# Kernel tuning notes

Measured on AMD Instinct MI355X. Metric: run time of the kernel, lower is better.

## Reference

```python
import jax, jax.numpy as jnp
from jax import lax
import numpy as np

DN = ('NCDHW', 'OIDHW', 'NCDHW')
SLOPE = 0.01   # nn.LeakyReLU default negative_slope
EPS = 1e-5     # nn.BatchNorm1d default eps


def _conv(x, w, s, p):
    return lax.conv_general_dilated(x, w, (s, s, s), [(p, p)] * 3,
                                    dimension_numbers=DN)


def _tconv(x, w):
    # ConvTranspose3d(k=4, s=2, p=1) == conv with lhs_dilation=2,
    # pad = k-1-p = 2, spatially flipped kernel. w is (C_out, C_in, 4,4,4).
    return lax.conv_general_dilated(x, jnp.flip(w, (2, 3, 4)), (1, 1, 1),
                                    [(2, 2)] * 3, lhs_dilation=(2, 2, 2),
                                    dimension_numbers=DN)


def _bcast(v):
    return v[None, :, None, None, None]


def _masked_bn(y, m, g, b):
    # BatchNorm1d over ACTIVE voxels only (spconv stores only active sites).
    cnt = jnp.maximum(jnp.sum(m), 1.0)
    mean = jnp.sum(y * m, axis=(0, 2, 3, 4)) / cnt
    var = jnp.sum(jnp.square(y - _bcast(mean)) * m, axis=(0, 2, 3, 4)) / cnt
    yhat = (y - _bcast(mean)) * _bcast(lax.rsqrt(var + EPS))
    return (yhat * _bcast(g) + _bcast(b)) * m


def _block(x, m, w, b, g, be, transpose):
    # spconv SparseConv(Transpose)3d -> LeakyReLU -> BatchNorm1d, emulated
    # densely: x is zero off the active set m; output active set is the
    # dilation of m by the kernel footprint; bias/activation/BN touch only
    # active sites.
    ones_k = jnp.ones((1, 1, 4, 4, 4), x.dtype)
    if transpose:
        y = _tconv(x, w)
        m2 = (_tconv(m, ones_k) > 0).astype(x.dtype)
    else:
        y = _conv(x, w, 2, 1)
        m2 = (_conv(m, ones_k, 2, 1) > 0).astype(x.dtype)
    y = (y + _bcast(b)) * m2
    y = jnp.where(y >= 0, y, SLOPE * y)  # LeakyReLU (preserves zeros)
    return _masked_bn(y, m2, g, be), m2


def setup_inputs() -> dict:
    key = jax.random.key(0)
    ks = jax.random.split(key, 16)
    B, C, D = 2, 4, 64
    c = 32          # chans
    pred_dim = 32

    def w_init(k, shape):
        scale = 1.0 / float(np.sqrt(np.prod(shape[1:])))
        return jax.random.normal(k, shape, jnp.float32) * scale

    def b_init(k, n):
        return jax.random.normal(k, (n,), jnp.float32) * 0.01

    inp = {
        'feat': jax.random.normal(ks[0], (B, C, D, D, D), jnp.float32),
        'mask': jax.random.uniform(ks[1], (B, 1, D, D, D), jnp.float32),
        # down: [C->c, c->2c, 2c->4c], k=4 s=2 p=1
        'w1': w_init(ks[2], (c, C, 4, 4, 4)),
        'b1': b_init(ks[3], c),
        'g1': jnp.ones((c,), jnp.float32), 'be1': jnp.zeros((c,), jnp.float32),
        'w2': w_init(ks[4], (2 * c, c, 4, 4, 4)),
        'b2': b_init(ks[5], 2 * c),
        'g2': jnp.ones((2 * c,), jnp.float32), 'be2': jnp.zeros((2 * c,), jnp.float32),
        'w3': w_init(ks[6], (4 * c, 2 * c, 4, 4, 4)),
        'b3': b_init(ks[7], 4 * c),
        'g3': jnp.ones((4 * c,), jnp.float32), 'be3': jnp.zeros((4 * c,), jnp.float32),
        # up: [4c->4c, 4c->2c] (no skip-concat in the executed forward)
        'tw1': w_init(ks[8], (4 * c, 4 * c, 4, 4, 4)),
        'tb1': b_init(ks[9], 4 * c),
        'tg1': jnp.ones((4 * c,), jnp.float32), 'tbe1': jnp.zeros((4 * c,), jnp.float32),
        'tw2': w_init(ks[10], (2 * c, 4 * c, 4, 4, 4)),
        'tb2': b_init(ks[11], 2 * c),
        'tg2': jnp.ones((2 * c,), jnp.float32), 'tbe2': jnp.zeros((2 * c,), jnp.float32),
        # final dense 1x1x1 Conv3d: 2c -> pred_dim
        'fw': w_init(ks[12], (pred_dim, 2 * c, 1, 1, 1)),
        'fb': b_init(ks[13], pred_dim),
    }
    return inp


def reference(feat, mask, w1, b1, g1, be1, w2, b2, g2, be2, w3, b3, g3, be3,
              tw1, tb1, tg1, tbe1, tw2, tb2, tg2, tbe2, fw, fb):
    m = (mask > 0.5).astype(feat.dtype)
    x = feat * m  # gather of active voxel features == dense zero-fill
    x, m = _block(x, m, w1, b1, g1, be1, False)   # 64^3 -> 32^3
    x, m = _block(x, m, w2, b2, g2, be2, False)   # 32^3 -> 16^3
    x, m = _block(x, m, w3, b3, g3, be3, False)   # 16^3 -> 8^3
    x, m = _block(x, m, tw1, tb1, tg1, tbe1, True)  # 8^3 -> 16^3
    x, m = _block(x, m, tw2, tb2, tg2, tbe2, True)  # 16^3 -> 32^3
    # ToDense() then dense 1x1x1 Conv3d (bias applied everywhere)
    return _conv(x, fw, 1, 0) + _bcast(fb)
```

## Files before the change

kernel.cpp:

```cpp
#include <hip/hip_runtime.h>
#include <hip/hip_bf16.h>

#define DEV static __device__ __forceinline__

typedef unsigned short ushort;
typedef __attribute__((ext_vector_type(8))) short short8;
typedef __attribute__((ext_vector_type(8))) ushort ushort8;
typedef __attribute__((ext_vector_type(4))) ushort ushortx4;
typedef __attribute__((ext_vector_type(4))) float accv;

DEV ushort f2bf(float f) {
    __hip_bfloat16 h = __float2bfloat16(f);
    return reinterpret_cast<ushort&>(h);
}

__device__ float    g_sred[5 * 128 * 32];
__device__ float    g_y1[2097152];
__device__ __align__(16) ushort g_y1b[2097152];
__device__ float    g_m1[65536];
__device__ float    g_y2[524288];
__device__ __align__(16) ushort g_y2b[524288];
__device__ float    g_m2[8192];
__device__ float    g_y3[131072];
__device__ __align__(16) ushort g_y3b[131072];
__device__ float    g_m3[1024];
__device__ float    g_t1[1048576];
__device__ __align__(16) ushort g_t1b[1048576];
__device__ float    g_mt1[8192];
__device__ float    g_mt2[65536];
__device__ float    g_t2[4194304];
__device__ __align__(16) ushort g_x0b[2097152];
__device__ float    g_p2[4194304];
__device__ float    g_p3[4194304];
__device__ float    g_p4[8388608];
__device__ __align__(16) ushort g_wb1[8192];
__device__ __align__(16) ushort g_wb2[131072];
__device__ __align__(16) ushort g_wb3[524288];
__device__ __align__(16) ushort g_wb4[1048576];
__device__ __align__(16) ushort g_wb5[524288];
__device__ float    g_fwt[2048];

__global__ __launch_bounds__(256)
void prep_all_kernel(const float* __restrict__ w1, const float* __restrict__ fw,
                     const float* __restrict__ w2, const float* __restrict__ w3,
                     const float* __restrict__ tw1, const float* __restrict__ tw2,
                     const float* __restrict__ feat, const float* __restrict__ mask) {
    int blk = blockIdx.x, tid = threadIdx.x;
    if (blk < 96) {
        int idx = blk * 256 + tid;
        if (idx < 20480) g_sred[idx] = 0.f;
        if (idx < 8192) {
            int co = idx >> 8, r = idx & 255;
            int tap = r >> 2, ci = r & 3;
            g_wb1[idx] = f2bf(w1[co * 256 + ci * 64 + tap]);
        }
        if (idx < 2048) { int co = idx >> 6, kg = idx & 63; g_fwt[kg * 32 + co] = fw[idx]; }
    } else if (blk < 608) {
        int idx = (blk - 96) * 256 + tid;
        int co = idx / 2048, r = idx % 2048;
        int ci = r >> 6, tap = r & 63;
        g_wb2[(size_t)co * 2048 + tap * 32 + ci] = f2bf(w2[idx]);
    } else if (blk < 2656) {
        int idx = (blk - 608) * 256 + tid;
        int co = idx / 4096, r = idx % 4096;
        int ci = r >> 6, tap = r & 63;
        g_wb3[(size_t)co * 4096 + tap * 64 + ci] = f2bf(w3[idx]);
    } else if (blk < 6752) {
        int idx = (blk - 2656) * 256 + tid;
        int co = idx / 8192, r = idx % 8192;
        int ci = r >> 6, t64 = r & 63;
        int kd = t64 >> 4, kh = (t64 >> 2) & 3, kw = t64 & 3;
        int pd = (3 - kd) & 1, td = (3 - kd) >> 1;
        int ph = (3 - kh) & 1, th = (3 - kh) >> 1;
        int pw = (3 - kw) & 1, tw = (3 - kw) >> 1;
        int parity = pd * 4 + ph * 2 + pw, t = td * 4 + th * 2 + tw;
        g_wb4[(((size_t)parity * 128 + co) * 8 + t) * 128 + ci] = f2bf(tw1[idx]);
    } else if (blk < 8800) {
        int idx = (blk - 6752) * 256 + tid;
        int co = idx / 8192, r = idx % 8192;
        int ci = r >> 6, t64 = r & 63;
        int kd = t64 >> 4, kh = (t64 >> 2) & 3, kw = t64 & 3;
        int pd = (3 - kd) & 1, td = (3 - kd) >> 1;
        int ph = (3 - kh) & 1, th = (3 - kh) >> 1;
        int pw = (3 - kw) & 1, tw = (3 - kw) >> 1;
        int parity = pd * 4 + ph * 2 + pw, t = td * 4 + th * 2 + tw;
        g_wb5[(((size_t)parity * 64 + co) * 8 + t) * 128 + ci] = f2bf(tw2[idx]);
    } else if (blk < 10848) {
        int idx = (blk - 8800) * 256 + tid;
        int b = idx >> 18, v = idx & 0x3FFFF;
        float mv = mask[idx] > 0.5f ? 1.f : 0.f;
        ushort pk[4];
#pragma unroll
        for (int c = 0; c < 4; c++) pk[c] = f2bf(feat[((b * 4 + c) << 18) + v] * mv);
        *(ushortx4*)&g_x0b[(size_t)idx * 4] = (ushortx4){pk[0], pk[1], pk[2], pk[3]};
    } else {
        int idx = (blk - 10848) * 256 + tid;
        int b = idx >> 15, v = idx & 0x7FFF;
        int od = v >> 10, rem = v & 1023;
        int oh = rem >> 5, ow = rem & 31;
        const float* mp = mask + ((size_t)b << 18);
        float acc = 0.f;
        for (int kd = 0; kd < 4; kd++) {
            int id = 2 * od - 1 + kd;
            if ((unsigned)id >= 64u) continue;
            for (int kh = 0; kh < 4; kh++) {
                int ih = 2 * oh - 1 + kh;
                if ((unsigned)ih >= 64u) continue;
                const float* row = mp + ((size_t)id * 64 + ih) * 64;
                for (int kw = 0; kw < 4; kw++) {
                    int iw = 2 * ow - 1 + kw;
                    if ((unsigned)iw < 64u && row[iw] > 0.5f) acc += 1.f;
                }
            }
        }
        g_m1[idx] = acc > 0.f ? 1.f : 0.f;
    }
}

DEV void mask_down_blk(const float* mprev, float* mout, int logDin, int logDo, int blk) {
    int Din = 1 << logDin, Do = 1 << logDo;
    int idx = blk * 256 + threadIdx.x;
    int b = idx >> (3 * logDo), v = idx & ((1 << (3 * logDo)) - 1);
    int od = v >> (2 * logDo), rem = v & ((1 << (2 * logDo)) - 1);
    int oh = rem >> logDo, ow = rem & (Do - 1);
    const float* mp = mprev + ((size_t)b << (3 * logDin));
    float acc = 0.f;
    for (int kd = 0; kd < 4; kd++) {
        int id = 2 * od - 1 + kd;
        if ((unsigned)id >= (unsigned)Din) continue;
        for (int kh = 0; kh < 4; kh++) {
            int ih = 2 * oh - 1 + kh;
            if ((unsigned)ih >= (unsigned)Din) continue;
            const float* row = mp + ((size_t)id * Din + ih) * Din;
            for (int kw = 0; kw < 4; kw++) {
                int iw = 2 * ow - 1 + kw;
                if ((unsigned)iw < (unsigned)Din) acc += row[iw];
            }
        }
    }
    mout[idx] = acc > 0.f ? 1.f : 0.f;
}

DEV void mask_up_blk(const float* mprev, float* mout, int logDin, int logDo, int blk) {
    int Din = 1 << logDin, Do = 1 << logDo;
    int idx = blk * 256 + threadIdx.x;
    int b = idx >> (3 * logDo), v = idx & ((1 << (3 * logDo)) - 1);
    int od = v >> (2 * logDo), rem = v & ((1 << (2 * logDo)) - 1);
    int oh = rem >> logDo, ow = rem & (Do - 1);
    const float* mp = mprev + ((size_t)b << (3 * logDin));
    float acc = 0.f;
    for (int kd = 0; kd < 4; kd++) {
        int u = od + kd - 2; if (u < 0 || (u & 1)) continue;
        int id = u >> 1; if (id >= Din) continue;
        for (int kh = 0; kh < 4; kh++) {
            int uh = oh + kh - 2; if (uh < 0 || (uh & 1)) continue;
            int ih = uh >> 1; if (ih >= Din) continue;
            const float* row = mp + ((size_t)id * Din + ih) * Din;
            for (int kw = 0; kw < 4; kw++) {
                int uw = ow + kw - 2; if (uw < 0 || (uw & 1)) continue;
                int iw = uw >> 1; if (iw >= Din) continue;
                acc += row[iw];
            }
        }
    }
    mout[idx] = acc > 0.f ? 1.f : 0.f;
}

template<int MODE, int MT, int NT, int CIN, int COUT, int LOGDI, int LOGDO, int SPLITK>
DEV void mfma_gemm_body(const ushort* __restrict__ xb, const ushort* __restrict__ wb,
                        float* __restrict__ y) {
    constexpr int KT = 32;
    constexpr int K  = (MODE == 1) ? CIN * 8 : CIN * 64;
    constexpr int KSEG = K / SPLITK;
    constexpr int LDA = 40;
    constexpr int MTW = MT / 32, NTW = NT / 32;
    constexpr int AR = MT * 4 / 256, BR = NT * 4 / 256;
    constexpr int LCIN = (CIN == 32) ? 5 : ((CIN == 64) ? 6 : 7);
    constexpr int Din = 1 << LOGDI, Do = 1 << LOGDO;
    constexpr int DvoxI = 1 << (3 * LOGDI), DvoxO = 1 << (3 * LOGDO);

    __shared__ __align__(16) ushort As[MT * LDA];
    __shared__ __align__(16) ushort Bs[NT * LDA];

    const int tid = threadIdx.x;
    const int bx = blockIdx.x;
    int pd = 0, ph = 0, pw = 0, ks = 0;
    const ushort* wp = wb;
    if constexpr (MODE == 1) {
        int z = blockIdx.z;
        pd = (z >> 2) & 1; ph = (z >> 1) & 1; pw = z & 1; ks = z >> 3;
        wp = wb + (size_t)(z & 7) * COUT * CIN * 8;
    } else {
        ks = blockIdx.z;
    }

    const int wv = tid >> 6, lane = tid & 63;
    const int mw = wv & 1, nw = wv >> 1;
    const int lr = lane & 15, quad = lane >> 4;

    int rB[BR], dB[BR], hB[BR], wBv[BR];
#pragma unroll
    for (int r = 0; r < BR; r++) {
        int slot = r * 256 + tid;
        int n = slot >> 2;
        int vg = bx * NT + n;
        if constexpr (MODE == 0) {
            rB[r] = vg >> (3 * LOGDO);
            int vv = vg & (DvoxO - 1);
            dB[r] = 2 * (vv >> (2 * LOGDO)) - 1;
            hB[r] = 2 * ((vv >> LOGDO) & (Do - 1)) - 1;
            wBv[r] = 2 * (vv & (Do - 1)) - 1;
        } else {
            rB[r] = vg >> (3 * LOGDI);
            int vv = vg & (DvoxI - 1);
            dB[r] = (vv >> (2 * LOGDI)) + pd - 1;
            hB[r] = ((vv >> LOGDI) & (Din - 1)) + ph - 1;
            wBv[r] = (vv & (Din - 1)) + pw - 1;
        }
    }

    auto gatherA = [&](int kt, ushort8* pa) {
#pragma unroll
        for (int r = 0; r < AR; r++) {
            int slot = r * 256 + tid;
            int m = slot >> 2, oct = slot & 3;
            pa[r] = *(const ushort8*)&wp[(size_t)m * K + kt + oct * 8];
        }
    };
    auto gatherB = [&](int kt, ushort8* pb) {
        int tap = kt >> LCIN;
        int cib = kt & (CIN - 1);
        int id_d, ih_d, iw_d;
        if constexpr (MODE == 0) { id_d = tap >> 4; ih_d = (tap >> 2) & 3; iw_d = tap & 3; }
        else                     { id_d = (tap >> 2) & 1; ih_d = (tap >> 1) & 1; iw_d = tap & 1; }
#pragma unroll
        for (int r = 0; r < BR; r++) {
            int oct = (r * 256 + tid) & 3;
            int ci0 = cib + oct * 8;
            int id = dB[r] + id_d, ih = hB[r] + ih_d, iw = wBv[r] + iw_d;
            ushort8 v = (ushort8){0, 0, 0, 0, 0, 0, 0, 0};
            if ((unsigned)id < (unsigned)Din && (unsigned)ih < (unsigned)Din &&
                (unsigned)iw < (unsigned)Din)
                v = *(const ushort8*)&xb[((size_t)rB[r] * DvoxI +
                                          (id << (2 * LOGDI)) + (ih << LOGDI) + iw) * CIN + ci0];
            pb[r] = v;
        }
    };

    accv acc[MTW][NTW];
#pragma unroll
    for (int mt = 0; mt < MTW; mt++)
#pragma unroll
        for (int nt = 0; nt < NTW; nt++) acc[mt][nt] = (accv){0.f, 0.f, 0.f, 0.f};

    const int kbeg = ks * KSEG, kend = kbeg + KSEG;
    ushort8 pa[AR], pb[BR], qa[AR], qb[BR];
    gatherA(kbeg, pa);
    gatherB(kbeg, pb);

    for (int kt = kbeg; kt < kend; kt += KT) {
        __syncthreads();
#pragma unroll
        for (int r = 0; r < AR; r++) {
            int slot = r * 256 + tid;
            int m = slot >> 2, oct = slot & 3;
            *(ushort8*)&As[m * LDA + oct * 8] = pa[r];
        }
#pragma unroll
        for (int r = 0; r < BR; r++) {
            int slot = r * 256 + tid;
            int n = slot >> 2, oct = slot & 3;
            *(ushort8*)&Bs[n * LDA + oct * 8] = pb[r];
        }
        __syncthreads();
        bool more = (kt + KT) < kend;
        if (more) { gatherA(kt + KT, qa); gatherB(kt + KT, qb); }

        short8 af[MTW], bfr[NTW];
#pragma unroll
        for (int mt = 0; mt < MTW; mt++)
            af[mt] = *(const short8*)&As[((mw * MTW + mt) * 16 + lr) * LDA + quad * 8];
#pragma unroll
        for (int nt = 0; nt < NTW; nt++)
            bfr[nt] = *(const short8*)&Bs[((nw * NTW + nt) * 16 + lr) * LDA + quad * 8];
#pragma unroll
        for (int mt = 0; mt < MTW; mt++)
#pragma unroll
            for (int nt = 0; nt < NTW; nt++)
                acc[mt][nt] = __builtin_amdgcn_mfma_f32_16x16x32_bf16(
                    af[mt], bfr[nt], acc[mt][nt], 0, 0, 0);
        if (more) {
#pragma unroll
            for (int r = 0; r < AR; r++) pa[r] = qa[r];
#pragma unroll
            for (int r = 0; r < BR; r++) pb[r] = qb[r];
        }
    }

    float* yp = y + (size_t)ks * (2 * COUT * DvoxO);
#pragma unroll
    for (int mt = 0; mt < MTW; mt++) {
#pragma unroll
        for (int nt = 0; nt < NTW; nt++) {
#pragma unroll
            for (int r = 0; r < 4; r++) {
                int co = (mw * MTW + mt) * 16 + quad * 4 + r;
                int vg = bx * NT + (nw * NTW + nt) * 16 + lr;
                size_t idx;
                if constexpr (MODE == 1) {
                    int b = vg >> (3 * LOGDI);
                    int vv = vg & (DvoxI - 1);
                    int odp = vv >> (2 * LOGDI), ohp = (vv >> LOGDI) & (Din - 1), owp = vv & (Din - 1);
                    int od = 2 * odp + pd, oh = 2 * ohp + ph, ow = 2 * owp + pw;
                    idx = (((size_t)(b * COUT + co)) << (3 * LOGDO)) +
                          (od << (2 * LOGDO)) + (oh << LOGDO) + ow;
                } else {
                    int b = vg >> (3 * LOGDO);
                    int off = vg & (DvoxO - 1);
                    idx = (((size_t)(b * COUT + co)) << (3 * LOGDO)) + off;
                }
                yp[idx] = acc[mt][nt][r];
            }
        }
    }
}

__global__ __launch_bounds__(256)
void conv2_kernel() { mfma_gemm_body<0, 64, 128, 32, 64, 5, 4, 8>(g_y1b, g_wb2, g_p2); }
__global__ __launch_bounds__(256)
void conv3_kernel() { mfma_gemm_body<0, 128, 64, 64, 128, 4, 3, 32>(g_y2b, g_wb3, g_p3); }
__global__ __launch_bounds__(256)
void conv4_kernel() { mfma_gemm_body<1, 128, 128, 128, 128, 3, 4, 8>(g_y3b, g_wb4, g_p4); }
__global__ __launch_bounds__(256)
void conv5_kernel() { mfma_gemm_body<1, 64, 128, 128, 64, 4, 5, 1>(g_t1b, g_wb5, g_t2); }

__global__ __launch_bounds__(256)
void conv1_kernel(const float* __restrict__ bias) {
    constexpr int LDA = 40;
    __shared__ __align__(16) ushort As[32 * LDA];
    __shared__ __align__(16) ushort Bs[64 * LDA];
    const int tid = threadIdx.x, bx = blockIdx.x;
    const int wv = tid >> 6, lane = tid & 63;
    const int lr = lane & 15, quad = lane >> 4;

    const int nB = tid >> 2, octB = tid & 3;
    const int vgB = bx * 64 + nB;
    const int bB = vgB >> 15, vB = vgB & 32767;
    const int odB = vB >> 10, ohB = (vB >> 5) & 31, owB = vB & 31;

    auto gatherA = [&](int kt, ushort8& pa) {
        if (tid < 128) {
            int m = tid >> 2, oct = tid & 3;
            pa = *(const ushort8*)&g_wb1[m * 256 + kt + oct * 8];
        }
    };
    auto gatherB = [&](int kt, ushort8& pb) {
        int kg0 = kt + octB * 8;
        int t0 = kg0 >> 2;
        int kd = t0 >> 4, kh = (t0 >> 2) & 3, kw0 = t0 & 3;
        int id = 2 * odB - 1 + kd;
        int ih = 2 * ohB - 1 + kh;
        int iw0 = 2 * owB - 1 + kw0;
        ushort8 v = (ushort8){0, 0, 0, 0, 0, 0, 0, 0};
        if ((unsigned)id < 64u && (unsigned)ih < 64u) {
            const ushort* base = g_x0b + ((((size_t)bB << 18) + (id << 12) + (ih << 6)) << 2);
            if (iw0 >= 0 && iw0 + 1 < 64) {
                v = *(const ushort8*)&base[iw0 << 2];
            } else {
                if ((unsigned)iw0 < 64u) {
                    ushortx4 h = *(const ushortx4*)&base[iw0 << 2];
                    v[0] = h[0]; v[1] = h[1]; v[2] = h[2]; v[3] = h[3];
                }
                if ((unsigned)(iw0 + 1) < 64u) {
                    ushortx4 h = *(const ushortx4*)&base[(iw0 + 1) << 2];
                    v[4] = h[0]; v[5] = h[1]; v[6] = h[2]; v[7] = h[3];
                }
            }
        }
        pb = v;
    };

    accv acc[2];
    acc[0] = (accv){0.f, 0.f, 0.f, 0.f};
    acc[1] = (accv){0.f, 0.f, 0.f, 0.f};
    ushort8 pa, pb, qa, qb;
    gatherA(0, pa); gatherB(0, pb);

    for (int kt = 0; kt < 256; kt += 32) {
        __syncthreads();
        if (tid < 128) { int m = tid >> 2, oct = tid & 3; *(ushort8*)&As[m * LDA + oct * 8] = pa; }
        *(ushort8*)&Bs[nB * LDA + octB * 8] = pb;
        __syncthreads();
        bool more = kt < 224;
        if (more) { gatherA(kt + 32, qa); gatherB(kt + 32, qb); }

        short8 b8 = *(const short8*)&Bs[(wv * 16 + lr) * LDA + quad * 8];
#pragma unroll
        for (int mt = 0; mt < 2; mt++) {
            short8 a8 = *(const short8*)&As[(mt * 16 + lr) * LDA + quad * 8];
            acc[mt] = __builtin_amdgcn_mfma_f32_16x16x32_bf16(a8, b8, acc[mt], 0, 0, 0);
        }
        if (more) { pa = qa; pb = qb; }
    }

#pragma unroll
    for (int mt = 0; mt < 2; mt++) {
#pragma unroll
        for (int r = 0; r < 4; r++) {
            int co = mt * 16 + quad * 4 + r;
            int vg = bx * 64 + wv * 16 + lr;
            int b = vg >> 15, off = vg & 32767;
            float mv = g_m1[((size_t)b << 15) + off];
            float yv = (acc[mt][r] + bias[co]) * mv;
            yv = yv >= 0.f ? yv : 0.01f * yv;
            g_y1[(((size_t)(b * 32 + co)) << 15) + off] = yv;
        }
    }
}

__global__ __launch_bounds__(256)
void final_kernel(const float* __restrict__ fb, const float* __restrict__ b5,
                  const float* __restrict__ tg2, const float* __restrict__ tbe2,
                  float* __restrict__ out) {
    __shared__ float As[1024];
    __shared__ float Bs[2048];
    __shared__ float sc5[64], sh5[64], bb5[64];
    const int tid = threadIdx.x, tc = tid & 15, tv = tid >> 4;
    const int bx = blockIdx.x;

    if (tid < 64) {
        const float* sred = g_sred + 16384;
        float n = fmaxf(sred[tid * 32 + 2], 1.f);
        float mean = sred[tid * 32] / n;
        float var = fmaxf(sred[tid * 32 + 1] / n - mean * mean, 0.f);
        float rstd = rsqrtf(var + 1e-5f);
        float s = tg2[tid] * rstd;
        sc5[tid] = s; sh5[tid] = tbe2[tid] - mean * s; bb5[tid] = b5[tid];
    }

    float acc[2][4] = {{0.f}};
    for (int kt = 0; kt < 64; kt += 32) {
        __syncthreads();
#pragma unroll
        for (int e = 0; e < 4; e++) As[e * 256 + tid] = g_fwt[kt * 32 + e * 256 + tid];
#pragma unroll
        for (int e = 0; e < 8; e++) {
            int j = e * 256 + tid;
            int kk = j >> 6, n = j & 63;
            int kg = kt + kk;
            int vg = bx * 64 + n;
            int b = vg >> 15, v = vg & 32767;
            float raw = g_t2[(((size_t)(b * 64 + kg)) << 15) + v];
            float mv = g_mt2[((size_t)b << 15) + v];
            float t = (raw + bb5[kg]) * mv;
            t = t >= 0.f ? t : 0.01f * t;
            Bs[kk * 64 + n] = (t * sc5[kg] + sh5[kg]) * mv;
        }
        __syncthreads();
#pragma unroll
        for (int kk = 0; kk < 32; kk++) {
            float2 a2 = *(const float2*)&As[kk * 32 + tc * 2];
            float4 b4 = *(const float4*)&Bs[kk * 64 + tv * 4];
            float a[2] = {a2.x, a2.y};
            float bb[4] = {b4.x, b4.y, b4.z, b4.w};
#pragma unroll
            for (int r = 0; r < 2; r++)
#pragma unroll
                for (int c = 0; c < 4; c++) acc[r][c] = fmaf(a[r], bb[c], acc[r][c]);
        }
    }
#pragma unroll
    for (int r = 0; r < 2; r++) {
        int co = tc * 2 + r;
        float bv = fb[co];
#pragma unroll
        for (int c = 0; c < 4; c++) {
            int vg = bx * 64 + tv * 4 + c;
            int b = vg >> 15, v = vg & 32767;
            out[(((size_t)(b * 32 + co)) << 15) + v] = acc[r][c] + bv;
        }
    }
}

DEV void red3_and_atomic(float s, float s2, float sm, float* sred, int co) {
#pragma unroll
    for (int off = 32; off; off >>= 1) {
        s  += __shfl_down(s, off, 64);
        s2 += __shfl_down(s2, off, 64);
        sm += __shfl_down(sm, off, 64);
    }
    __shared__ float red[12];
    int lane = threadIdx.x & 63, wvi = threadIdx.x >> 6;
    if (!lane) { red[wvi] = s; red[4 + wvi] = s2; red[8 + wvi] = sm; }
    __syncthreads();
    if (!threadIdx.x) {
        atomicAdd(&sred[co * 32 + 0], red[0] + red[1] + red[2] + red[3]);
        atomicAdd(&sred[co * 32 + 1], red[4] + red[5] + red[6] + red[7]);
        atomicAdd(&sred[co * 32 + 2], red[8] + red[9] + red[10] + red[11]);
    }
}

template<int COUT, int LOGDO, int SPLITK, int ITERS, bool WRITE>
DEV void post_body(const float* __restrict__ bias, const float* __restrict__ m2,
                   const float* p, float* y, float* sred) {
    constexpr int Dvox = 1 << (3 * LOGDO);
    constexpr size_t STR = (size_t)2 * COUT * Dvox;
    constexpr int LOGC = (COUT == 128) ? 7 : ((COUT == 64) ? 6 : 5);
    int base = blockIdx.x * (ITERS * 256);
    int co = (base >> (3 * LOGDO)) & (COUT - 1);
    float s = 0.f, s2 = 0.f, sm = 0.f;
#pragma unroll
    for (int it = 0; it < ITERS; it++) {
        int idx = base + it * 256 + threadIdx.x;
        int v = idx & (Dvox - 1);
        int b = idx >> (3 * LOGDO + LOGC);
        float sum = 0.f;
#pragma unroll
        for (int k = 0; k < SPLITK; k++) sum += p[k * STR + idx];
        float mv = m2[((size_t)b << (3 * LOGDO)) + v];
        float yv = (sum + bias[co]) * mv;
        yv = yv >= 0.f ? yv : 0.01f * yv;
        if constexpr (WRITE) y[idx] = yv;
        s += yv; s2 += yv * yv; sm += mv;
    }
    red3_and_atomic(s, s2, sm, sred, co);
}

__global__ __launch_bounds__(256) void post2_kernel(const float* b) { post_body<64, 4, 8, 1, true>(b, g_m2, g_p2, g_y2, g_sred + 4096); }
__global__ __launch_bounds__(256) void post3_kernel(const float* b) { post_body<128, 3, 32, 1, true>(b, g_m3, g_p3, g_y3, g_sred + 8192); }
__global__ __launch_bounds__(256) void post4_kernel(const float* b) { post_body<128, 4, 8, 2, true>(b, g_mt1, g_p4, g_t1, g_sred + 12288); }
__global__ __launch_bounds__(256) void post5_kernel(const float* b) { post_body<64, 5, 1, 8, false>(b, g_mt2, g_t2, g_t2, g_sred + 16384); }

__global__ __launch_bounds__(256)
void stats1_kernel() {
    int base = blockIdx.x * 1024;
    int co = (base >> 15) & 31;
    float s = 0.f, s2 = 0.f, sm = 0.f;
#pragma unroll
    for (int it = 0; it < 4; it++) {
        int idx = base + it * 256 + threadIdx.x;
        int v = idx & 32767;
        int b = idx >> 20;
        float yv = g_y1[idx];
        float mv = g_m1[((size_t)b << 15) + v];
        s += yv; s2 += yv * yv; sm += mv;
    }
    red3_and_atomic(s, s2, sm, g_sred, co);
}

template<int LOGC, int LOGD>
DEV void bn_fused_body(const float* __restrict__ y, ushort* __restrict__ out,
                       const float* __restrict__ sred, const float* __restrict__ gm,
                       const float* __restrict__ be, const float* __restrict__ m2,
                       int blk) {
    constexpr int C = 1 << LOGC, Dvox = 1 << LOGD;
    __shared__ float sc[C], sh[C];
    int tid = threadIdx.x;
    if (tid < C) {
        float n = fmaxf(sred[tid * 32 + 2], 1.f);
        float mean = sred[tid * 32] / n;
        float var = fmaxf(sred[tid * 32 + 1] / n - mean * mean, 0.f);
        float rstd = rsqrtf(var + 1e-5f);
        float s = gm[tid] * rstd;
        sc[tid] = s; sh[tid] = be[tid] - mean * s;
    }
    __syncthreads();
    int gv = blk * 256 + tid;
    int b = gv >> LOGD, vox = gv & (Dvox - 1);
    float mv = m2[gv];
    const float* yp = y + (((size_t)b << LOGC) << LOGD) + vox;
    ushort* op = out + (size_t)gv * C;
#pragma unroll
    for (int c0 = 0; c0 < C; c0 += 8) {
        ushort pk[8];
#pragma unroll
        for (int j = 0; j < 8; j++) {
            int c = c0 + j;
            float val = yp[(size_t)c << LOGD];
            pk[j] = f2bf((val * sc[c] + sh[c]) * mv);
        }
        *(ushort8*)&op[c0] = (ushort8){pk[0], pk[1], pk[2], pk[3], pk[4], pk[5], pk[6], pk[7]};
    }
}

__global__ __launch_bounds__(256)
void bn1_kernel(const float* g, const float* be) {
    if (blockIdx.x < 256) bn_fused_body<5, 15>(g_y1, g_y1b, g_sred + 0, g, be, g_m1, blockIdx.x);
    else mask_down_blk(g_m1, g_m2, 5, 4, blockIdx.x - 256);
}
__global__ __launch_bounds__(256)
void bn2_kernel(const float* g, const float* be) {
    if (blockIdx.x < 32) bn_fused_body<6, 12>(g_y2, g_y2b, g_sred + 4096, g, be, g_m2, blockIdx.x);
    else mask_down_blk(g_m2, g_m3, 4, 3, blockIdx.x - 32);
}
__global__ __launch_bounds__(256)
void bn3_kernel(const float* g, const float* be) {
    if (blockIdx.x < 4) bn_fused_body<7, 9>(g_y3, g_y3b, g_sred + 8192, g, be, g_m3, blockIdx.x);
    else mask_up_blk(g_m3, g_mt1, 3, 4, blockIdx.x - 4);
}
__global__ __launch_bounds__(256)
void bn4_kernel(const float* g, const float* be) {
    if (blockIdx.x < 32) bn_fused_body<7, 12>(g_t1, g_t1b, g_sred + 12288, g, be, g_mt1, blockIdx.x);
    else mask_up_blk(g_mt1, g_mt2, 4, 5, blockIdx.x - 32);
}


extern "C" void kernel_launch(void* const* d_in, const int* in_sizes, int n_in,
                              void* d_out, int out_size, void* d_ws, size_t ws_size,
                              hipStream_t stream) {
    (void)in_sizes; (void)n_in; (void)out_size; (void)d_ws; (void)ws_size;
    const float* feat = (const float*)d_in[0];
    const float* mask = (const float*)d_in[1];
    const float* w1  = (const float*)d_in[2];
    const float* b1  = (const float*)d_in[3];
    const float* g1  = (const float*)d_in[4];
    const float* be1 = (const float*)d_in[5];
    const float* w2  = (const float*)d_in[6];
    const float* b2  = (const float*)d_in[7];
    const float* g2  = (const float*)d_in[8];
    const float* be2 = (const float*)d_in[9];
    const float* w3  = (const float*)d_in[10];
    const float* b3  = (const float*)d_in[11];
    const float* g3  = (const float*)d_in[12];
    const float* be3 = (const float*)d_in[13];
    const float* tw1 = (const float*)d_in[14];
    const float* tb1 = (const float*)d_in[15];
    const float* tg1 = (const float*)d_in[16];
    const float* tbe1= (const float*)d_in[17];
    const float* tw2 = (const float*)d_in[18];
    const float* tb2 = (const float*)d_in[19];
    const float* tg2 = (const float*)d_in[20];
    const float* tbe2= (const float*)d_in[21];
    const float* fw  = (const float*)d_in[22];
    const float* fb  = (const float*)d_in[23];

    prep_all_kernel<<<11104, 256, 0, stream>>>(w1, fw, w2, w3, tw1, tw2, feat, mask);

    conv1_kernel<<<1024, 256, 0, stream>>>(b1);
    stats1_kernel<<<2048, 256, 0, stream>>>();
    bn1_kernel<<<288, 256, 0, stream>>>(g1, be1);

    conv2_kernel<<<dim3(64, 1, 8), 256, 0, stream>>>();
    post2_kernel<<<2048, 256, 0, stream>>>(b2);
    bn2_kernel<<<36, 256, 0, stream>>>(g2, be2);

    conv3_kernel<<<dim3(16, 1, 32), 256, 0, stream>>>();
    post3_kernel<<<512, 256, 0, stream>>>(b3);
    bn3_kernel<<<36, 256, 0, stream>>>(g3, be3);

    conv4_kernel<<<dim3(8, 1, 64), 256, 0, stream>>>();
    post4_kernel<<<2048, 256, 0, stream>>>(tb1);
    bn4_kernel<<<288, 256, 0, stream>>>(tg1, tbe1);

    conv5_kernel<<<dim3(64, 1, 8), 256, 0, stream>>>();
    post5_kernel<<<2048, 256, 0, stream>>>(tb2);

    final_kernel<<<1024, 256, 0, stream>>>(fb, tb2, tg2, tbe2, (float*)d_out);
}
```

Baseline: 278.3 us.

## Fuse BN stats into conv epilogues, load weights directly to registers, reduce split-K

Removes the separate stats1 and post5 kernels by computing the masked sum, sum-of-squares and mask count inside the conv1 and conv5 epilogues. Partial sums go through shuffle reduction and shared-memory atomics before global atomics. Weight tiles are now loaded straight from global memory into MFMA operand registers instead of being staged through LDS. Split-K for conv3 and conv4 is halved, which shrinks the partial buffers the post kernels must sum, at the cost of fewer blocks in flight.

```diff
diff --git a/kernel.cpp b/kernel.cpp
--- a/kernel.cpp
+++ b/kernel.cpp
@@ -166,21 +166,25 @@
     mout[idx] = acc > 0.f ? 1.f : 0.f;
 }
 
-template<int MODE, int MT, int NT, int CIN, int COUT, int LOGDI, int LOGDO, int SPLITK>
+template<int MODE, int MT, int NT, int CIN, int COUT, int LOGDI, int LOGDO, int SPLITK,
+         bool STATS = false>
 DEV void mfma_gemm_body(const ushort* __restrict__ xb, const ushort* __restrict__ wb,
-                        float* __restrict__ y) {
+                        float* __restrict__ y,
+                        const float* __restrict__ bias = nullptr,
+                        const float* __restrict__ m2 = nullptr,
+                        float* __restrict__ sred = nullptr) {
     constexpr int KT = 32;
     constexpr int K  = (MODE == 1) ? CIN * 8 : CIN * 64;
     constexpr int KSEG = K / SPLITK;
     constexpr int LDA = 40;
     constexpr int MTW = MT / 32, NTW = NT / 32;
-    constexpr int AR = MT * 4 / 256, BR = NT * 4 / 256;
+    constexpr int BR = NT * 4 / 256;
     constexpr int LCIN = (CIN == 32) ? 5 : ((CIN == 64) ? 6 : 7);
     constexpr int Din = 1 << LOGDI, Do = 1 << LOGDO;
     constexpr int DvoxI = 1 << (3 * LOGDI), DvoxO = 1 << (3 * LOGDO);
 
-    __shared__ __align__(16) ushort As[MT * LDA];
     __shared__ __align__(16) ushort Bs[NT * LDA];
+    __shared__ float st[STATS ? COUT * 3 : 1];
 
     const int tid = threadIdx.x;
     const int bx = blockIdx.x;
@@ -197,6 +201,10 @@
     const int wv = tid >> 6, lane = tid & 63;
     const int mw = wv & 1, nw = wv >> 1;
     const int lr = lane & 15, quad = lane >> 4;
+
+    if constexpr (STATS) {
+        for (int i = tid; i < COUT * 3; i += 256) st[i] = 0.f;
+    }
 
     int rB[BR], dB[BR], hB[BR], wBv[BR];
 #pragma unroll
@@ -219,12 +227,11 @@
         }
     }
 
-    auto gatherA = [&](int kt, ushort8* pa) {
-#pragma unroll
-        for (int r = 0; r < AR; r++) {
-            int slot = r * 256 + tid;
-            int m = slot >> 2, oct = slot & 3;
-            pa[r] = *(const ushort8*)&wp[(size_t)m * K + kt + oct * 8];
+    auto loadA = [&](int kt, short8* a) {
+#pragma unroll
+        for (int mt = 0; mt < MTW; mt++) {
+            int m = (mw * MTW + mt) * 16 + lr;
+            a[mt] = *(const short8*)&wp[(size_t)m * K + kt + quad * 8];
         }
     };
     auto gatherB = [&](int kt, ushort8* pb) {
@@ -254,18 +261,13 @@
         for (int nt = 0; nt < NTW; nt++) acc[mt][nt] = (accv){0.f, 0.f, 0.f, 0.f};
 
     const int kbeg = ks * KSEG, kend = kbeg + KSEG;
-    ushort8 pa[AR], pb[BR], qa[AR], qb[BR];
-    gatherA(kbeg, pa);
+    ushort8 pb[BR], qb[BR];
+    short8 paf[MTW], qaf[MTW];
     gatherB(kbeg, pb);
+    loadA(kbeg, paf);
 
     for (int kt = kbeg; kt < kend; kt += KT) {
         __syncthreads();
-#pragma unroll
-        for (int r = 0; r < AR; r++) {
-            int slot = r * 256 + tid;
-            int m = slot >> 2, oct = slot & 3;
-            *(ushort8*)&As[m * LDA + oct * 8] = pa[r];
-        }
 #pragma unroll
         for (int r = 0; r < BR; r++) {
             int slot = r * 256 + tid;
@@ -274,12 +276,9 @@
         }
         __syncthreads();
         bool more = (kt + KT) < kend;
-        if (more) { gatherA(kt + KT, qa); gatherB(kt + KT, qb); }
-
-        short8 af[MTW], bfr[NTW];
-#pragma unroll
-        for (int mt = 0; mt < MTW; mt++)
-            af[mt] = *(const short8*)&As[((mw * MTW + mt) * 16 + lr) * LDA + quad * 8];
+        if (more) { gatherB(kt + KT, qb); loadA(kt + KT, qaf); }
+
+        short8 bfr[NTW];
 #pragma unroll
         for (int nt = 0; nt < NTW; nt++)
             bfr[nt] = *(const short8*)&Bs[((nw * NTW + nt) * 16 + lr) * LDA + quad * 8];
@@ -288,39 +287,94 @@
 #pragma unroll
             for (int nt = 0; nt < NTW; nt++)
                 acc[mt][nt] = __builtin_amdgcn_mfma_f32_16x16x32_bf16(
-                    af[mt], bfr[nt], acc[mt][nt], 0, 0, 0);
+                    paf[mt], bfr[nt], acc[mt][nt], 0, 0, 0);
         if (more) {
 #pragma unroll
-            for (int r = 0; r < AR; r++) pa[r] = qa[r];
-#pragma unroll
             for (int r = 0; r < BR; r++) pb[r] = qb[r];
+#pragma unroll
+            for (int mt = 0; mt < MTW; mt++) paf[mt] = qaf[mt];
         }
     }
 
     float* yp = y + (size_t)ks * (2 * COUT * DvoxO);
-#pragma unroll
-    for (int mt = 0; mt < MTW; mt++) {
-#pragma unroll
-        for (int nt = 0; nt < NTW; nt++) {
+    float sacc[MTW][4], s2acc[MTW][4], bco[MTW][4];
+    float mvs = 0.f;
+    if constexpr (STATS) {
+#pragma unroll
+        for (int mt = 0; mt < MTW; mt++)
+#pragma unroll
+            for (int r = 0; r < 4; r++) {
+                sacc[mt][r] = 0.f; s2acc[mt][r] = 0.f;
+                bco[mt][r] = bias[(mw * MTW + mt) * 16 + quad * 4 + r];
+            }
+    }
+#pragma unroll
+    for (int nt = 0; nt < NTW; nt++) {
+        int vg = bx * NT + (nw * NTW + nt) * 16 + lr;
+        int b, vvox;
+        if constexpr (MODE == 1) {
+            b = vg >> (3 * LOGDI);
+            int vv = vg & (DvoxI - 1);
+            int odp = vv >> (2 * LOGDI), ohp = (vv >> LOGDI) & (Din - 1), owp = vv & (Din - 1);
+            vvox = ((2 * odp + pd) << (2 * LOGDO)) + ((2 * ohp + ph) << LOGDO) + (2 * owp + pw);
+        } else {
+            b = vg >> (3 * LOGDO);
+            vvox = vg & (DvoxO - 1);
+        }
+        float mv = 0.f;
+        if constexpr (STATS) {
+            mv = m2[((size_t)b << (3 * LOGDO)) + vvox];
+            mvs += mv;
+        }
+        size_t base = (((size_t)b * COUT) << (3 * LOGDO)) + vvox;
+#pragma unroll
+        for (int mt = 0; mt < MTW; mt++) {
 #pragma unroll
             for (int r = 0; r < 4; r++) {
                 int co = (mw * MTW + mt) * 16 + quad * 4 + r;
-                int vg = bx * NT + (nw * NTW + nt) * 16 + lr;
-                size_t idx;
-                if constexpr (MODE == 1) {
-                    int b = vg >> (3 * LOGDI);
-                    int vv = vg & (DvoxI - 1);
-                    int odp = vv >> (2 * LOGDI), ohp = (vv >> LOGDI) & (Din - 1), owp = vv & (Din - 1);
-                    int od = 2 * odp + pd, oh = 2 * ohp + ph, ow = 2 * owp + pw;
-                    idx = (((size_t)(b * COUT + co)) << (3 * LOGDO)) +
-                          (od << (2 * LOGDO)) + (oh << LOGDO) + ow;
-                } else {
-                    int b = vg >> (3 * LOGDO);
-                    int off = vg & (DvoxO - 1);
-                    idx = (((size_t)(b * COUT + co)) << (3 * LOGDO)) + off;
+                float v = acc[mt][nt][r];
+                yp[base + ((size_t)co << (3 * LOGDO))] = v;
+                if constexpr (STATS) {
+                    float yv = (v + bco[mt][r]) * mv;
+                    yv = yv >= 0.f ? yv : 0.01f * yv;
+                    sacc[mt][r] += yv; s2acc[mt][r] += yv * yv;
                 }
-                yp[idx] = acc[mt][nt][r];
-            }
+            }
+        }
+    }
+
+    if constexpr (STATS) {
+#pragma unroll
+        for (int mt = 0; mt < MTW; mt++)
+#pragma unroll
+            for (int r = 0; r < 4; r++) {
+                float s = sacc[mt][r], s2 = s2acc[mt][r];
+#pragma unroll
+                for (int o = 8; o; o >>= 1) {
+                    s  += __shfl_xor(s, o, 16);
+                    s2 += __shfl_xor(s2, o, 16);
+                }
+                if (lr == 0) {
+                    int co = (mw * MTW + mt) * 16 + quad * 4 + r;
+                    atomicAdd(&st[co * 3 + 0], s);
+                    atomicAdd(&st[co * 3 + 1], s2);
+                }
+            }
+        float ms = mvs;
+#pragma unroll
+        for (int o = 8; o; o >>= 1) ms += __shfl_xor(ms, o, 16);
+        if (lr == 0) {
+#pragma unroll
+            for (int mt = 0; mt < MTW; mt++)
+#pragma unroll
+                for (int r = 0; r < 4; r++)
+                    atomicAdd(&st[((mw * MTW + mt) * 16 + quad * 4 + r) * 3 + 2], ms);
+        }
+        __syncthreads();
+        for (int i = tid; i < COUT; i += 256) {
+            atomicAdd(&sred[i * 32 + 0], st[i * 3 + 0]);
+            atomicAdd(&sred[i * 32 + 1], st[i * 3 + 1]);
+            atomicAdd(&sred[i * 32 + 2], st[i * 3 + 2]);
         }
     }
 }
@@ -328,31 +382,35 @@
 __global__ __launch_bounds__(256)
 void conv2_kernel() { mfma_gemm_body<0, 64, 128, 32, 64, 5, 4, 8>(g_y1b, g_wb2, g_p2); }
 __global__ __launch_bounds__(256)
-void conv3_kernel() { mfma_gemm_body<0, 128, 64, 64, 128, 4, 3, 32>(g_y2b, g_wb3, g_p3); }
-__global__ __launch_bounds__(256)
-void conv4_kernel() { mfma_gemm_body<1, 128, 128, 128, 128, 3, 4, 8>(g_y3b, g_wb4, g_p4); }
-__global__ __launch_bounds__(256)
-void conv5_kernel() { mfma_gemm_body<1, 64, 128, 128, 64, 4, 5, 1>(g_t1b, g_wb5, g_t2); }
+void conv3_kernel() { mfma_gemm_body<0, 128, 64, 64, 128, 4, 3, 16>(g_y2b, g_wb3, g_p3); }
+__global__ __launch_bounds__(256)
+void conv4_kernel() { mfma_gemm_body<1, 128, 128, 128, 128, 3, 4, 4>(g_y3b, g_wb4, g_p4); }
+__global__ __launch_bounds__(256)
+void conv5_kernel(const float* __restrict__ b5) {
+    mfma_gemm_body<1, 64, 128, 128, 64, 4, 5, 1, true>(g_t1b, g_wb5, g_t2,
+                                                       b5, g_mt2, g_sred + 16384);
+}
 
 __global__ __launch_bounds__(256)
 void conv1_kernel(const float* __restrict__ bias) {
     constexpr int LDA = 40;
-    __shared__ __align__(16) ushort As[32 * LDA];
     __shared__ __align__(16) ushort Bs[64 * LDA];
+    __shared__ float st[96];
     const int tid = threadIdx.x, bx = blockIdx.x;
     const int wv = tid >> 6, lane = tid & 63;
     const int lr = lane & 15, quad = lane >> 4;
+
+    if (tid < 96) st[tid] = 0.f;
 
     const int nB = tid >> 2, octB = tid & 3;
     const int vgB = bx * 64 + nB;
     const int bB = vgB >> 15, vB = vgB & 32767;
     const int odB = vB >> 10, ohB = (vB >> 5) & 31, owB = vB & 31;
 
-    auto gatherA = [&](int kt, ushort8& pa) {
-        if (tid < 128) {
-            int m = tid >> 2, oct = tid & 3;
-            pa = *(const ushort8*)&g_wb1[m * 256 + kt + oct * 8];
-        }
+    auto loadA = [&](int kt, short8* a) {
+#pragma unroll
+        for (int mt = 0; mt < 2; mt++)
+            a[mt] = *(const short8*)&g_wb1[(mt * 16 + lr) * 256 + kt + quad * 8];
     };
     auto gatherB = [&](int kt, ushort8& pb) {
         int kg0 = kt + octB * 8;
@@ -383,38 +441,71 @@
     accv acc[2];
     acc[0] = (accv){0.f, 0.f, 0.f, 0.f};
     acc[1] = (accv){0.f, 0.f, 0.f, 0.f};
-    ushort8 pa, pb, qa, qb;
-    gatherA(0, pa); gatherB(0, pb);
+    ushort8 pb, qb;
+    short8 pa2[2], qa2[2];
+    gatherB(0, pb); loadA(0, pa2);
 
     for (int kt = 0; kt < 256; kt += 32) {
         __syncthreads();
-        if (tid < 128) { int m = tid >> 2, oct = tid & 3; *(ushort8*)&As[m * LDA + oct * 8] = pa; }
         *(ushort8*)&Bs[nB * LDA + octB * 8] = pb;
         __syncthreads();
         bool more = kt < 224;
-        if (more) { gatherA(kt + 32, qa); gatherB(kt + 32, qb); }
+        if (more) { gatherB(kt + 32, qb); loadA(kt + 32, qa2); }
 
         short8 b8 = *(const short8*)&Bs[(wv * 16 + lr) * LDA + quad * 8];
 #pragma unroll
-        for (int mt = 0; mt < 2; mt++) {
-            short8 a8 = *(const short8*)&As[(mt * 16 + lr) * LDA + quad * 8];
-            acc[mt] = __builtin_amdgcn_mfma_f32_16x16x32_bf16(a8, b8, acc[mt], 0, 0, 0);
-        }
-        if (more) { pa = qa; pb = qb; }
-    }
-
+        for (int mt = 0; mt < 2; mt++)
+            acc[mt] = __builtin_amdgcn_mfma_f32_16x16x32_bf16(pa2[mt], b8, acc[mt], 0, 0, 0);
+        if (more) { pb = qb; pa2[0] = qa2[0]; pa2[1] = qa2[1]; }
+    }
+
+    int vg = bx * 64 + wv * 16 + lr;
+    int b = vg >> 15, off = vg & 32767;
+    float mv = g_m1[((size_t)b << 15) + off];
+    float sacc[2][4], s2acc[2][4];
 #pragma unroll
     for (int mt = 0; mt < 2; mt++) {
 #pragma unroll
         for (int r = 0; r < 4; r++) {
             int co = mt * 16 + quad * 4 + r;
-            int vg = bx * 64 + wv * 16 + lr;
-            int b = vg >> 15, off = vg & 32767;
-            float mv = g_m1[((size_t)b << 15) + off];
             float yv = (acc[mt][r] + bias[co]) * mv;
             yv = yv >= 0.f ? yv : 0.01f * yv;
             g_y1[(((size_t)(b * 32 + co)) << 15) + off] = yv;
-        }
+            sacc[mt][r] = yv; s2acc[mt][r] = yv * yv;
+        }
+    }
+#pragma unroll
+    for (int mt = 0; mt < 2; mt++) {
+#pragma unroll
+        for (int r = 0; r < 4; r++) {
+            float s = sacc[mt][r], s2 = s2acc[mt][r];
+#pragma unroll
+            for (int o = 8; o; o >>= 1) {
+                s  += __shfl_xor(s, o, 16);
+                s2 += __shfl_xor(s2, o, 16);
+            }
+            if (lr == 0) {
+                int co = mt * 16 + quad * 4 + r;
+                atomicAdd(&st[co * 3 + 0], s);
+                atomicAdd(&st[co * 3 + 1], s2);
+            }
+        }
+    }
+    float ms = mv;
+#pragma unroll
+    for (int o = 8; o; o >>= 1) ms += __shfl_xor(ms, o, 16);
+    if (lr == 0) {
+#pragma unroll
+        for (int mt = 0; mt < 2; mt++)
+#pragma unroll
+            for (int r = 0; r < 4; r++)
+                atomicAdd(&st[(mt * 16 + quad * 4 + r) * 3 + 2], ms);
+    }
+    __syncthreads();
+    if (tid < 32) {
+        atomicAdd(&g_sred[tid * 32 + 0], st[tid * 3 + 0]);
+        atomicAdd(&g_sred[tid * 32 + 1], st[tid * 3 + 1]);
+        atomicAdd(&g_sred[tid * 32 + 2], st[tid * 3 + 2]);
     }
 }
 
@@ -527,26 +618,8 @@
 }
 
 __global__ __launch_bounds__(256) void post2_kernel(const float* b) { post_body<64, 4, 8, 1, true>(b, g_m2, g_p2, g_y2, g_sred + 4096); }
-__global__ __launch_bounds__(256) void post3_kernel(const float* b) { post_body<128, 3, 32, 1, true>(b, g_m3, g_p3, g_y3, g_sred + 8192); }
-__global__ __launch_bounds__(256) void post4_kernel(const float* b) { post_body<128, 4, 8, 2, true>(b, g_mt1, g_p4, g_t1, g_sred + 12288); }
-__global__ __launch_bounds__(256) void post5_kernel(const float* b) { post_body<64, 5, 1, 8, false>(b, g_mt2, g_t2, g_t2, g_sred + 16384); }
-
-__global__ __launch_bounds__(256)
-void stats1_kernel() {
-    int base = blockIdx.x * 1024;
-    int co = (base >> 15) & 31;
-    float s = 0.f, s2 = 0.f, sm = 0.f;
-#pragma unroll
-    for (int it = 0; it < 4; it++) {
-        int idx = base + it * 256 + threadIdx.x;
-        int v = idx & 32767;
-        int b = idx >> 20;
-        float yv = g_y1[idx];
-        float mv = g_m1[((size_t)b << 15) + v];
-        s += yv; s2 += yv * yv; sm += mv;
-    }
-    red3_and_atomic(s, s2, sm, g_sred, co);
-}
+__global__ __launch_bounds__(256) void post3_kernel(const float* b) { post_body<128, 3, 16, 1, true>(b, g_m3, g_p3, g_y3, g_sred + 8192); }
+__global__ __launch_bounds__(256) void post4_kernel(const float* b) { post_body<128, 4, 4, 2, true>(b, g_mt1, g_p4, g_t1, g_sred + 12288); }
 
 template<int LOGC, int LOGD>
 DEV void bn_fused_body(const float* __restrict__ y, ushort* __restrict__ out,
@@ -637,23 +710,21 @@
     prep_all_kernel<<<11104, 256, 0, stream>>>(w1, fw, w2, w3, tw1, tw2, feat, mask);
 
     conv1_kernel<<<1024, 256, 0, stream>>>(b1);
-    stats1_kernel<<<2048, 256, 0, stream>>>();
     bn1_kernel<<<288, 256, 0, stream>>>(g1, be1);
 
     conv2_kernel<<<dim3(64, 1, 8), 256, 0, stream>>>();
     post2_kernel<<<2048, 256, 0, stream>>>(b2);
     bn2_kernel<<<36, 256, 0, stream>>>(g2, be2);
 
-    conv3_kernel<<<dim3(16, 1, 32), 256, 0, stream>>>();
+    conv3_kernel<<<dim3(16, 1, 16), 256, 0, stream>>>();
     post3_kernel<<<512, 256, 0, stream>>>(b3);
     bn3_kernel<<<36, 256, 0, stream>>>(g3, be3);
 
-    conv4_kernel<<<dim3(8, 1, 64), 256, 0, stream>>>();
+    conv4_kernel<<<dim3(8, 1, 32), 256, 0, stream>>>();
     post4_kernel<<<2048, 256, 0, stream>>>(tb1);
     bn4_kernel<<<288, 256, 0, stream>>>(tg1, tbe1);
 
-    conv5_kernel<<<dim3(64, 1, 8), 256, 0, stream>>>();
-    post5_kernel<<<2048, 256, 0, stream>>>(tb2);
+    conv5_kernel<<<dim3(64, 1, 8), 256, 0, stream>>>(tb2);
 
     final_kernel<<<1024, 256, 0, stream>>>(fb, tb2, tg2, tbe2, (float*)d_out);
 }
```

Measured after the change: 325.7 us. +17.0%, slower.
